# Kernel optimization log

Measured on AMD Instinct MI355X. Metric: run time of the kernel, lower is better.

Reference implementation:

```python
import jax, jax.numpy as jnp
import numpy as np

B, T, C = 4, 1024, 2048
H, N = 32, 64
D_DECAY, D_AAA, D_MV, D_GATE = 96, 96, 64, 256


def setup_inputs() -> dict:
    key = jax.random.key(0)
    ks = iter(jax.random.split(key, 48))

    def rn(shape, s):
        return jax.random.normal(next(ks), shape, jnp.float32) * s

    inp = {
        "x": rn((B, T, C), 1.0),
        "shift_state_in": rn((B, C), 1.0),
        "wkv_state_in": jnp.zeros((B, H, N, N), jnp.float32),
        "v_first_val": rn((B, T, C), 1.0),
    }
    for nme in ["x_r", "x_w", "x_k", "x_v", "x_a", "x_g"]:
        inp[nme] = rn((C,), 0.2) + 0.5
    inp["w0"] = rn((C,), 0.3) - 4.0  # log-log decay bias, keeps decay in (0,1)
    inp["w1"] = rn((C, D_DECAY), 0.02)
    inp["w2"] = rn((D_DECAY, C), 0.02)
    inp["a0"] = rn((C,), 0.1)
    inp["a1"] = rn((C, D_AAA), 0.02)
    inp["a2"] = rn((D_AAA, C), 0.02)
    inp["v0"] = jnp.ones((C,), jnp.float32)
    inp["v1"] = rn((C, D_MV), 0.02)
    inp["v2"] = rn((D_MV, C), 0.02)
    inp["g1"] = rn((C, D_GATE), 0.02)
    inp["g2"] = rn((D_GATE, C), 0.02)
    inp["k_k"] = jnp.full((C,), 0.85, jnp.float32)
    inp["k_a"] = jnp.ones((C,), jnp.float32)
    inp["r_k"] = rn((H, N), 0.02)
    s = 1.0 / float(np.sqrt(C))
    for nme in ["Wr", "Wk", "Wv", "Wo"]:
        inp[nme] = rn((C, C), s)
    inp["ln_w"] = jnp.ones((C,), jnp.float32)
    inp["ln_b"] = jnp.zeros((C,), jnp.float32)
    return inp


def _forward(x, shift_state_in, wkv_state_in, v_first_val,
             x_r, x_w, x_k, x_v, x_a, x_g,
             w0, w1, w2, a0, a1, a2, v0, v1, v2, g1, g2,
             k_k, k_a, r_k, Wr, Wk, Wv, Wo, ln_w, ln_b):
    Bs, Ts, Cs = x.shape
    shift_state_out = x[:, -1]
    # token shift
    xprev = jnp.concatenate([shift_state_in[:, None, :], x[:, :-1]], axis=1)
    dx = xprev - x
    xr = x + dx * x_r
    xw = x + dx * x_w
    xk = x + dx * x_k
    xv = x + dx * x_v
    xa = x + dx * x_a
    xg = x + dx * x_g
    r = xr @ Wr.T
    k = xk @ Wk.T
    v = xv @ Wv.T
    # soft-clamped log-log decay: w in (-inf, -0.5], decay = exp(-exp(w)) in (0,1)
    w_log = -jax.nn.softplus(-(w0 + jnp.tanh(xw @ w1) @ w2)) - 0.5
    decay = jnp.exp(-jnp.exp(w_log))
    a = jax.nn.sigmoid(a0 + (xa @ a1) @ a2)  # in-context learning rate
    g = jax.nn.sigmoid(xg @ g1) @ g2          # output gate
    # removal key: per-head L2-normalized
    kk = (k * k_k).reshape(Bs, Ts, H, N)
    kk = kk / jnp.maximum(jnp.linalg.norm(kk, axis=-1, keepdims=True), 1e-12)
    kk = kk.reshape(Bs, Ts, Cs)
    k = k * (1.0 + (a - 1.0) * k_a)
    # layer_id > 0: value residual mixing with first-layer values
    v = v + (v_first_val - v) * jax.nn.sigmoid(v0 + (xv @ v1) @ v2)
    v_first_out = v_first_val

    # [B,T,C] -> [T,B,H,N] for scan
    def th(t):
        return t.reshape(Bs, Ts, H, N).transpose(1, 0, 2, 3)

    r_s, w_s, k_s, v_s, kk_s, a_s = map(th, (r, decay, k, v, kk, a))

    def step(state, inp):
        rt, wt, kt, vt, kkt, at = inp  # each [B,H,N]
        # state: [B,H,N_value,N_key]
        sab = jnp.einsum('bhvn,bhn,bhm->bhvm', state, -kkt, kkt * at)
        state = state * wt[:, :, None, :] + sab + vt[..., None] * kt[:, :, None, :]
        yt = jnp.einsum('bhvn,bhn->bhv', state, rt)
        return state, yt

    wkv_state_out, y = jax.lax.scan(step, wkv_state_in, (r_s, w_s, k_s, v_s, kk_s, a_s))
    y = y.transpose(1, 0, 2, 3)  # [B,T,H,N]

    # GroupNorm over each head (eps = 1e-5 * head_size)
    eps = 1e-5 * N
    mu = y.mean(-1, keepdims=True)
    var = y.var(-1, keepdims=True)
    yn = (y - mu) / jnp.sqrt(var + eps)
    yn = yn * ln_w.reshape(H, N) + ln_b.reshape(H, N)
    yn = yn.reshape(Bs, Ts, Cs)

    rr = r.reshape(Bs, Ts, H, N)
    kh = k.reshape(Bs, Ts, H, N)
    vh = v.reshape(Bs, Ts, H, N)
    bonus = ((rr * kh * r_k).sum(-1, keepdims=True) * vh).reshape(Bs, Ts, Cs)
    out = ((yn + bonus) * g) @ Wo.T
    return out, shift_state_out, wkv_state_out, v_first_out


def reference(x, shift_state_in, wkv_state_in, v_first_val,
              x_r, x_w, x_k, x_v, x_a, x_g,
              w0, w1, w2, a0, a1, a2, v0, v1, v2, g1, g2,
              k_k, k_a, r_k, Wr, Wk, Wv, Wo, ln_w, ln_b):
    return _forward(x, shift_state_in, wkv_state_in, v_first_val,
                    x_r, x_w, x_k, x_v, x_a, x_g,
                    w0, w1, w2, a0, a1, a2, v0, v1, v2, g1, g2,
                    k_k, k_a, r_k, Wr, Wk, Wv, Wo, ln_w, ln_b)
```

## Files before the change

kernel.cpp:

```cpp
#include <hip/hip_runtime.h>
#include <hip/hip_bf16.h>
#include <stdint.h>

typedef unsigned short u16;
typedef unsigned int u32;
typedef unsigned long long u64;
typedef __attribute__((ext_vector_type(8))) short short8;
typedef __attribute__((ext_vector_type(4))) float f32x4;
typedef __attribute__((ext_vector_type(2))) unsigned int u32x2;

#define BB 4
#define TT 1024
#define CC 2048

__device__ __forceinline__ u16 f2bf(float f){
  __hip_bfloat16 h = __float2bfloat16(f);
  return *reinterpret_cast<u16*>(&h);
}
__device__ __forceinline__ float bf2f(u16 h){
  union { u32 u; float f; } v; v.u = ((u32)h) << 16; return v.f;
}
__device__ __forceinline__ float bflo(u32 p){
  union { u32 u; float f; } v; v.u = p << 16; return v.f;
}
__device__ __forceinline__ float bfhi(u32 p){
  union { u32 u; float f; } v; v.u = p & 0xFFFF0000u; return v.f;
}

__device__ __forceinline__ void gload16(const void* g, void* s){
  __builtin_amdgcn_global_load_lds((const __attribute__((address_space(1))) u32*)g,
                                   (__attribute__((address_space(3))) u32*)s, 16, 0, 0);
}

__device__ __forceinline__ float wave_sum64(float x){
  #pragma unroll
  for (int m = 1; m < 64; m <<= 1) x += __shfl_xor(x, m, 64);
  return x;
}

template<int N>
__device__ __forceinline__ float ror_add(float x){
  int t = __builtin_amdgcn_update_dpp(0, __builtin_bit_cast(int, x), 0x120 | N, 0xF, 0xF, false);
  return x + __builtin_bit_cast(float, t);
}
__device__ __forceinline__ float red16(float x){
  x = ror_add<8>(x); x = ror_add<4>(x); x = ror_add<2>(x); x = ror_add<1>(x);
  return x;
}

__device__ __forceinline__ void xcd_map(int nx, int& bx, int& row0){
  const int G = gridDim.x;
  const int q = G >> 3, r = G & 7;
  const int xcd = blockIdx.x & 7, i2 = blockIdx.x >> 3;
  const int sw = (xcd < r) ? (xcd*(q+1) + i2) : (r*(q+1) + (xcd - r)*q + i2);
  const int by = sw / nx;
  bx = sw - by*nx;
  row0 = by * 128;
}

__global__ __launch_bounds__(256) void k_wprep(
  const float* __restrict__ wr, const float* __restrict__ wk,
  const float* __restrict__ wv, const float* __restrict__ wo,
  const float* __restrict__ w1, const float* __restrict__ a1,
  const float* __restrict__ v1, const float* __restrict__ g1,
  const float* __restrict__ w2, const float* __restrict__ a2,
  const float* __restrict__ v2, const float* __restrict__ g2,
  u16* __restrict__ wsb)
{
  __shared__ float lds[32][33];
  const int blk0 = blockIdx.x;
  if (blk0 < 16384){
    int i = blk0*256 + threadIdx.x;
    int seg = i >> 20;
    int off = (i & 1048575) * 4;
    const float* src = (seg==0) ? wr : (seg==1) ? wk : (seg==2) ? wv : wo;
    const size_t dofs = (seg==0) ? 4194304u : (seg==1) ? 8388608u : (seg==2) ? 12582912u : 0u;
    float4 v = *(const float4*)&src[off];
    *(ushort4*)&wsb[dofs + off] = make_ushort4(f2bf(v.x), f2bf(v.y), f2bf(v.z), f2bf(v.w));
    return;
  }
  const int blk = blk0 - 16384;
  const float* src; int R, S, Rpad, tile, tiles_r; size_t dst;
  if      (blk <  256){ src=w1; R=2048; S=96;   Rpad=2048; dst=16777216u; tile=blk;      tiles_r=64; }
  else if (blk <  512){ src=a1; R=2048; S=96;   Rpad=2048; dst=17039360u; tile=blk-256;  tiles_r=64; }
  else if (blk <  768){ src=v1; R=2048; S=64;   Rpad=2048; dst=17301504u; tile=blk-512;  tiles_r=64; }
  else if (blk < 1280){ src=g1; R=2048; S=256;  Rpad=2048; dst=17563648u; tile=blk-768;  tiles_r=64; }
  else if (blk < 1536){ src=w2; R=96;   S=2048; Rpad=128;  dst=18087936u; tile=blk-1280; tiles_r=4;  }
  else if (blk < 1792){ src=a2; R=96;   S=2048; Rpad=128;  dst=18350080u; tile=blk-1536; tiles_r=4;  }
  else if (blk < 2048){ src=v2; R=64;   S=2048; Rpad=128;  dst=18612224u; tile=blk-1792; tiles_r=4;  }
  else                { src=g2; R=256;  S=2048; Rpad=256;  dst=18874368u; tile=blk-2048; tiles_r=8;  }
  const int tr = tile % tiles_r, ts = tile / tiles_r;
  const int r0 = tr*32, s0 = ts*32;
  const int tj = threadIdx.x & 31, ti = threadIdx.x >> 5;
  #pragma unroll
  for (int p=0;p<4;p++){
    int rr = r0 + p*8 + ti, ss = s0 + tj;
    lds[p*8+ti][tj] = (rr < R && ss < S) ? src[(size_t)rr*S + ss] : 0.f;
  }
  __syncthreads();
  #pragma unroll
  for (int p=0;p<4;p++){
    int sl = p*8 + ti, rl = tj;
    wsb[dst + (size_t)(s0+sl)*Rpad + r0 + rl] = f2bf(lds[rl][sl]);
  }
}

__global__ __launch_bounds__(256) void k_prep4(
  const float* __restrict__ x, const float* __restrict__ shift_in,
  const float* __restrict__ mr, const float* __restrict__ mk,
  const float* __restrict__ mv, const float* __restrict__ mw,
  u16* __restrict__ xr, u16* __restrict__ xk, u16* __restrict__ xv, u16* __restrict__ xw)
{
  int idx = blockIdx.x*256 + threadIdx.x;
  int c4 = (idx & 511) * 4;
  int t  = (idx >> 9) & (TT-1);
  int b  = idx >> 19;
  size_t xo = ((size_t)(b*TT + t))*CC + c4;
  float4 xc = *(const float4*)&x[xo];
  float4 xp = (t == 0) ? *(const float4*)&shift_in[(size_t)b*CC + c4]
                       : *(const float4*)&x[xo - CC];
  float d0 = xp.x-xc.x, d1 = xp.y-xc.y, d2 = xp.z-xc.z, d3 = xp.w-xc.w;
#define MIXO(mp, op) { float4 m = *(const float4*)&mp[c4]; \
    *(ushort4*)&op[xo] = make_ushort4(f2bf(fmaf(d0,m.x,xc.x)), f2bf(fmaf(d1,m.y,xc.y)), \
                                      f2bf(fmaf(d2,m.z,xc.z)), f2bf(fmaf(d3,m.w,xc.w))); }
  MIXO(mr, xr); MIXO(mk, xk); MIXO(mv, xv); MIXO(mw, xw);
#undef MIXO
}

template<int AMODE>
__device__ __forceinline__ void gemm_body(
  const u16* __restrict__ Abf,
  const float* __restrict__ xg, const float* __restrict__ shiftg,
  const float* __restrict__ ma, const float* __restrict__ mg,
  const u16* __restrict__ Bt, float* __restrict__ Cf, u16* __restrict__ Cb,
  int K, int lda, int ldb, int ldc, int nx)
{
  __shared__ alignas(16) u16 sA[128*32];
  __shared__ alignas(16) u16 sB[128*32];
  const int tid = threadIdx.x;
  const int wv = tid >> 6, ln = tid & 63;
  int bx, row0;
  xcd_map(nx, bx, row0);
  const int wr = wv >> 1, wc = wv & 1;

  const float* mixv = nullptr;
  const u16* Ap = Abf;
  const u16* Btp = Bt;
  u16* Cbp = Cb;
  bool bmix = false;
  int bcol0 = bx * 128;
  int ccol0 = bx * 128;
  int ldaa = lda, ldbb = ldb, ldcc = ldc;
  int KK = K, act = 0;

  if (AMODE == 2){
    if (bx < 48){
      int sel = bx >> 4;
      Ap = Abf + (size_t)sel * 8388608u;
      Cbp = Cb + (size_t)sel * 8388608u;
      ccol0 = (bx & 15) * 128;
      ldcc = 2048; ldaa = 2048;
    } else {
      int sb = bx - 48;
      Cbp = (u16*)Cf;
      ccol0 = sb * 128;
      ldcc = 640;
      act = (sb==0) ? 1 : (sb>=3 ? 2 : 0);
      if (sb == 0){ Ap = Abf + 25165824u; ldaa = 2048; }
      else if (sb == 2){ Ap = Abf + 16777216u; ldaa = 2048; }
      else { bmix = true; mixv = (sb==1) ? ma : mg; }
    }
  }
  if (AMODE == 3){
    int sel = bx >> 4;
    Ap = Abf + sel*128;
    Btp = Bt + (size_t)sel * 262144u;
    ldbb = (sel==3) ? 256 : 128;
    KK = (sel==3) ? 256 : 128;
    const int coffs[4] = {0, 8388608, 17842176, 26230784};
    Cbp = Cb + coffs[sel];
    ccol0 = (bx & 15) * 128;
    bcol0 = ccol0;
    ldcc = 2048;
  }

  f32x4 acc[4][4] = {};
  const int ob0 = wv*2048;
  const int o0  = ob0 + ln*16;
  const int rA0 = o0 >> 6;
  const int ke0 = (o0 & 63) >> 1;
  const int ar  = tid >> 2;
  const int akc = (tid & 3) * 8;

  for (int k0 = 0; k0 < KK; k0 += 32){
    __syncthreads();
    if (AMODE != 2 || !bmix){
      gload16(&Ap[(size_t)(row0 + rA0     )*ldaa + k0 + ke0], (void*)((char*)sA + ob0));
      gload16(&Ap[(size_t)(row0 + rA0 + 16)*ldaa + k0 + ke0], (void*)((char*)sA + ob0 + 1024));
    }
    gload16(&Btp[(size_t)(bcol0 + rA0     )*ldbb + k0 + ke0], (void*)((char*)sB + ob0));
    gload16(&Btp[(size_t)(bcol0 + rA0 + 16)*ldbb + k0 + ke0], (void*)((char*)sB + ob0 + 1024));
    if (AMODE == 2 && bmix){
      float4 m0 = *(const float4*)&mixv[k0 + akc];
      float4 m1 = *(const float4*)&mixv[k0 + akc + 4];
      #pragma unroll
      for (int it = 0; it < 2; ++it){
        int r = ar + it*64;
        int gr = row0 + r;
        size_t xo = (size_t)gr*CC + k0 + akc;
        float4 c0 = *(const float4*)&xg[xo];
        float4 c1 = *(const float4*)&xg[xo + 4];
        const float* pp = ((gr & (TT-1)) == 0) ? &shiftg[(size_t)(gr >> 10)*CC + k0 + akc]
                                               : &xg[xo - CC];
        float4 p0 = *(const float4*)&pp[0];
        float4 p1 = *(const float4*)&pp[4];
        short8 vvv;
        vvv[0] = (short)f2bf(c0.x + (p0.x - c0.x)*m0.x);
        vvv[1] = (short)f2bf(c0.y + (p0.y - c0.y)*m0.y);
        vvv[2] = (short)f2bf(c0.z + (p0.z - c0.z)*m0.z);
        vvv[3] = (short)f2bf(c0.w + (p0.w - c0.w)*m0.w);
        vvv[4] = (short)f2bf(c1.x + (p1.x - c1.x)*m1.x);
        vvv[5] = (short)f2bf(c1.y + (p1.y - c1.y)*m1.y);
        vvv[6] = (short)f2bf(c1.z + (p1.z - c1.z)*m1.z);
        vvv[7] = (short)f2bf(c1.w + (p1.w - c1.w)*m1.w);
        *(short8*)&sA[r*32 + akc] = vvv;
      }
    }
    __syncthreads();
    short8 aF[4], bF[4];
    #pragma unroll
    for (int m=0;m<4;m++) aF[m] = *(const short8*)&sA[(wr*64 + m*16 + (ln&15))*32 + (ln>>4)*8];
    #pragma unroll
    for (int n=0;n<4;n++) bF[n] = *(const short8*)&sB[(wc*64 + n*16 + (ln&15))*32 + (ln>>4)*8];
    #pragma unroll
    for (int m=0;m<4;m++)
      #pragma unroll
      for (int n=0;n<4;n++)
        acc[m][n] = __builtin_amdgcn_mfma_f32_16x16x32_bf16(aF[m], bF[n], acc[m][n], 0,0,0);
  }

  const int cr = (ln >> 4) * 4, ccol = ln & 15;
  #pragma unroll
  for (int m=0;m<4;m++){
    #pragma unroll
    for (int n=0;n<4;n++){
      int gc = ccol0 + wc*64 + n*16 + ccol;
      #pragma unroll
      for (int j=0;j<4;j++){
        int gr = row0 + wr*64 + m*16 + cr + j;
        float v = acc[m][n][j];
        if (AMODE == 0){
          Cf[(size_t)gr*ldcc + gc] = v;
        } else {
          if (act == 1) v = tanhf(v);
          else if (act == 2) v = 1.f/(1.f + expf(-v));
          Cbp[(size_t)gr*ldcc + gc] = f2bf(v);
        }
      }
    }
  }
}

__global__ __launch_bounds__(256) void k_gemm_rkv(
  const u16* Abf, const float* xg, const float* shiftg, const float* ma, const float* mg,
  const u16* Bt, float* Cf, u16* Cb, int K, int lda, int ldb, int ldc, int nx)
{ gemm_body<2>(Abf, xg, shiftg, ma, mg, Bt, Cf, Cb, K, lda, ldb, ldc, nx); }

__global__ __launch_bounds__(256) void k_gemm_s2(
  const u16* Abf, const float* xg, const float* shiftg, const float* ma, const float* mg,
  const u16* Bt, float* Cf, u16* Cb, int K, int lda, int ldb, int ldc, int nx)
{ gemm_body<3>(Abf, xg, shiftg, ma, mg, Bt, Cf, Cb, K, lda, ldb, ldc, nx); }

__global__ __launch_bounds__(256) void k_gemm_fin(
  const u16* Abf, const float* xg, const float* shiftg, const float* ma, const float* mg,
  const u16* Bt, float* Cf, u16* Cb, int K, int lda, int ldb, int ldc, int nx)
{ gemm_body<0>(Abf, xg, shiftg, ma, mg, Bt, Cf, Cb, K, lda, ldb, ldc, nx); }

__global__ __launch_bounds__(256) void k_post1(
  u16* __restrict__ kb, u16* __restrict__ vb, const u16* __restrict__ winb,
  u16* __restrict__ ainb, u16* __restrict__ vinb,
  const float* __restrict__ vfirst,
  const float* __restrict__ w0, const float* __restrict__ a0, const float* __restrict__ v0,
  const float* __restrict__ kkv, const float* __restrict__ kav,
  float* __restrict__ dec)
{
  int grp = blockIdx.x*4 + (threadIdx.x >> 6);
  int n = threadIdx.x & 63;
  int i = grp >> 5, h = grp & 31;
  int c = h*64 + n;
  size_t idx = (size_t)i*CC + c;
  float k  = bf2f(kb[idx]),  v = bf2f(vb[idx]);
  float wi = bf2f(winb[idx]), ai = bf2f(ainb[idx]), vi = bf2f(vinb[idx]);
  float vf = vfirst[idx];
  float a  = 1.f/(1.f + expf(-(a0[c] + ai)));
  float z  = -(w0[c] + wi);
  float sp = (z > 15.f) ? z : log1pf(expf(z));
  float decay = expf(-expf(-sp - 0.5f));
  float vg = 1.f/(1.f + expf(-(v0[c] + vi)));
  float vfin = v + (vf - v)*vg;
  float kkr = k * kkv[c];
  float ss = wave_sum64(kkr*kkr);
  float kkn = kkr / fmaxf(sqrtf(ss), 1e-12f);
  float kfin = k * (1.f + (a - 1.f)*kav[c]);
  kb[idx] = f2bf(kfin);
  vb[idx] = f2bf(vfin);
  dec[idx] = decay;
  vinb[idx] = f2bf(kkn);
  ainb[idx] = f2bf(-(kkn * a));
}

#define SDECL(S) float4 w##S[8]; u32x2 b##S[8], k##S[8], kk##S[8], r##S[8]; u32 v##S[8];

#define SISSUE(S, t0) do {                                                        \
  _Pragma("unroll")                                                               \
  for (int s_=0; s_<8; ++s_){                                                     \
    u64 ow = (u64)(uintptr_t)&wb [gc0 + (size_t)((t0)+s_)*CC];                    \
    u64 ob = (u64)(uintptr_t)&bbp[gc0 + (size_t)((t0)+s_)*CC];                    \
    u64 ok = (u64)(uintptr_t)&kb [gc0 + (size_t)((t0)+s_)*CC];                    \
    u64 oq = (u64)(uintptr_t)&kkb[gc0 + (size_t)((t0)+s_)*CC];                    \
    u64 orr= (u64)(uintptr_t)&rb [gc0 + (size_t)((t0)+s_)*CC];                    \
    u64 ov = (u64)(uintptr_t)&vb [gv0 + (size_t)((t0)+s_)*CC];                    \
    asm volatile("global_load_dwordx4 %0, %1, off" : "=v"(w##S[s_])  : "v"(ow) : "memory"); \
    asm volatile("global_load_dwordx2 %0, %1, off" : "=v"(b##S[s_])  : "v"(ob) : "memory"); \
    asm volatile("global_load_dwordx2 %0, %1, off" : "=v"(k##S[s_])  : "v"(ok) : "memory"); \
    asm volatile("global_load_dwordx2 %0, %1, off" : "=v"(kk##S[s_]) : "v"(oq) : "memory"); \
    asm volatile("global_load_dwordx2 %0, %1, off" : "=v"(r##S[s_])  : "v"(orr): "memory"); \
    asm volatile("global_load_dword   %0, %1, off" : "=v"(v##S[s_])  : "v"(ov) : "memory"); \
  }                                                                               \
} while(0)

#define SCHUNK(S, t0, CNT) do {                                                   \
  asm volatile("s_waitcnt vmcnt(" #CNT ")" ::: "memory");                         \
  __builtin_amdgcn_sched_barrier(0);                                              \
  _Pragma("unroll")                                                               \
  for (int s_=0; s_<8; ++s_){                                                     \
    const float w_0=w##S[s_].x, w_1=w##S[s_].y, w_2=w##S[s_].z, w_3=w##S[s_].w;   \
    const float b_0=bflo(b##S[s_].x), b_1=bfhi(b##S[s_].x),                       \
                b_2=bflo(b##S[s_].y), b_3=bfhi(b##S[s_].y);                       \
    const float k_0=bflo(k##S[s_].x), k_1=bfhi(k##S[s_].x),                       \
                k_2=bflo(k##S[s_].y), k_3=bfhi(k##S[s_].y);                       \
    const float q_0=bflo(kk##S[s_].x), q_1=bfhi(kk##S[s_].x),                     \
                q_2=bflo(kk##S[s_].y), q_3=bfhi(kk##S[s_].y);                     \
    const float r_0=bflo(r##S[s_].x), r_1=bfhi(r##S[s_].x),                       \
                r_2=bflo(r##S[s_].y), r_3=bfhi(r##S[s_].y);                       \
    const float vv0_ = bflo(v##S[s_]);                                            \
    const float vv1_ = bfhi(v##S[s_]);                                            \
    float p0_ = fmaf(st[0][0],q_0, st[0][1]*q_1) + fmaf(st[0][2],q_2, st[0][3]*q_3); \
    float p1_ = fmaf(st[1][0],q_0, st[1][1]*q_1) + fmaf(st[1][2],q_2, st[1][3]*q_3); \
    p0_ = red16(p0_); p1_ = red16(p1_);                                           \
    st[0][0] = fmaf(st[0][0],w_0, fmaf(p0_,b_0, vv0_*k_0));                       \
    st[0][1] = fmaf(st[0][1],w_1, fmaf(p0_,b_1, vv0_*k_1));                       \
    st[0][2] = fmaf(st[0][2],w_2, fmaf(p0_,b_2, vv0_*k_2));                       \
    st[0][3] = fmaf(st[0][3],w_3, fmaf(p0_,b_3, vv0_*k_3));                       \
    st[1][0] = fmaf(st[1][0],w_0, fmaf(p1_,b_0, vv1_*k_0));                       \
    st[1][1] = fmaf(st[1][1],w_1, fmaf(p1_,b_1, vv1_*k_1));                       \
    st[1][2] = fmaf(st[1][2],w_2, fmaf(p1_,b_2, vv1_*k_2));                       \
    st[1][3] = fmaf(st[1][3],w_3, fmaf(p1_,b_3, vv1_*k_3));                       \
    float y0_ = fmaf(st[0][0],r_0, st[0][1]*r_1) + fmaf(st[0][2],r_2, st[0][3]*r_3); \
    float y1_ = fmaf(st[1][0],r_0, st[1][1]*r_1) + fmaf(st[1][2],r_2, st[1][3]*r_3); \
    y0_ = red16(y0_); y1_ = red16(y1_);                                           \
    if (cg == 0){                                                                 \
      u32 pk_ = (u32)f2bf(y0_) | ((u32)f2bf(y1_) << 16);                          \
      *(u32*)&yb[gv0 + (size_t)((t0)+s_)*CC] = pk_;                               \
    }                                                                             \
  }                                                                               \
} while(0)

__global__ __launch_bounds__(64, 1) void k_scan(
  const u16* __restrict__ rb, const float* __restrict__ wb,
  const u16* __restrict__ kb, const u16* __restrict__ vb,
  const u16* __restrict__ kkb, const u16* __restrict__ bbp,
  const float* __restrict__ wkv_in, u16* __restrict__ yb, float* __restrict__ wkv_out)
{
  const int blk = blockIdx.x;
  const int bh = blk & 127, oct = blk >> 7;
  const int b = bh >> 5, h = bh & 31;
  const int ln = threadIdx.x;
  const int rg = ln >> 4;
  const int cg = ln & 15;
  const int row0 = oct*8 + rg*2;
  const int col0 = cg*4;

  float st[2][4];
  {
    const float* sp0 = &wkv_in[((size_t)bh*64 + row0    )*64 + col0];
    const float* sp1 = &wkv_in[((size_t)bh*64 + row0 + 1)*64 + col0];
    float4 a = *(const float4*)sp0, c = *(const float4*)sp1;
    st[0][0]=a.x; st[0][1]=a.y; st[0][2]=a.z; st[0][3]=a.w;
    st[1][0]=c.x; st[1][1]=c.y; st[1][2]=c.z; st[1][3]=c.w;
  }

  const size_t gc0 = ((size_t)b*TT)*CC + h*64 + col0;
  const size_t gv0 = ((size_t)b*TT)*CC + h*64 + row0;

  SDECL(A) SDECL(B)

  SISSUE(A, 0);
  SISSUE(B, 8);
  SCHUNK(A, 0, 48);
  SISSUE(A, 16);
  SCHUNK(B, 8, 56);
  SISSUE(B, 24);
  for (int c = 1; c < 63; ++c){
    const int t0 = c*16;
    SCHUNK(A, t0, 56);
    SISSUE(A, t0+16);
    SCHUNK(B, t0+8, 56);
    SISSUE(B, t0+24);
  }
  SCHUNK(A, 1008, 56);
  SCHUNK(B, 1016, 0);

  {
    float* wo0 = &wkv_out[((size_t)bh*64 + row0    )*64 + col0];
    float* wo1 = &wkv_out[((size_t)bh*64 + row0 + 1)*64 + col0];
    *(float4*)wo0 = make_float4(st[0][0], st[0][1], st[0][2], st[0][3]);
    *(float4*)wo1 = make_float4(st[1][0], st[1][1], st[1][2], st[1][3]);
  }
}

__global__ __launch_bounds__(256) void k_post2(
  const u16* __restrict__ ybuf, const u16* __restrict__ rbuf,
  const u16* __restrict__ kfb, const u16* __restrict__ vfb,
  const u16* __restrict__ gbuf, const float* __restrict__ rk,
  const float* __restrict__ lnw, const float* __restrict__ lnb, u16* __restrict__ ao)
{
  int grp = blockIdx.x*4 + (threadIdx.x >> 6);
  int n = threadIdx.x & 63;
  int i = grp >> 5, h = grp & 31;
  int c = h*64 + n;
  size_t idx = (size_t)i*CC + c;
  float y = bf2f(ybuf[idx]);
  float s1 = wave_sum64(y);
  float s2 = wave_sum64(y*y);
  float mu = s1 * (1.f/64.f);
  float var = s2 * (1.f/64.f) - mu*mu;
  float yn = (y - mu) * rsqrtf(var + 6.4e-4f) * lnw[c] + lnb[c];
  float rv = bf2f(rbuf[idx]), kv = bf2f(kfb[idx]);
  float s3 = wave_sum64(rv * kv * rk[c]);
  float bonus = s3 * bf2f(vfb[idx]);
  ao[idx] = f2bf((yn + bonus) * bf2f(gbuf[idx]));
}

__global__ __launch_bounds__(256) void k_shift(const float* __restrict__ x, float* __restrict__ so){
  int i = blockIdx.x*256 + threadIdx.x;
  int b = i >> 9, c4 = (i & 511)*4;
  *(float4*)&so[(size_t)b*CC + c4] = *(const float4*)&x[((size_t)(b*TT + TT-1))*CC + c4];
}

extern "C" void kernel_launch(void* const* d_in, const int* in_sizes, int n_in,
                              void* d_out, int out_size, void* d_ws, size_t ws_size,
                              hipStream_t stream)
{
  const float* x        = (const float*)d_in[0];
  const float* shift_in = (const float*)d_in[1];
  const float* wkv_in   = (const float*)d_in[2];
  const float* v_first  = (const float*)d_in[3];
  const float* x_r = (const float*)d_in[4];
  const float* x_w = (const float*)d_in[5];
  const float* x_k = (const float*)d_in[6];
  const float* x_v = (const float*)d_in[7];
  const float* x_a = (const float*)d_in[8];
  const float* x_g = (const float*)d_in[9];
  const float* w0 = (const float*)d_in[10];
  const float* w1 = (const float*)d_in[11];
  const float* w2 = (const float*)d_in[12];
  const float* a0 = (const float*)d_in[13];
  const float* a1 = (const float*)d_in[14];
  const float* a2 = (const float*)d_in[15];
  const float* v0 = (const float*)d_in[16];
  const float* v1 = (const float*)d_in[17];
  const float* v2 = (const float*)d_in[18];
  const float* g1 = (const float*)d_in[19];
  const float* g2 = (const float*)d_in[20];
  const float* k_k = (const float*)d_in[21];
  const float* k_a = (const float*)d_in[22];
  const float* r_k = (const float*)d_in[23];
  const float* Wr = (const float*)d_in[24];
  const float* Wk = (const float*)d_in[25];
  const float* Wv = (const float*)d_in[26];
  const float* Wo = (const float*)d_in[27];
  const float* ln_w = (const float*)d_in[28];
  const float* ln_b = (const float*)d_in[29];

  char* ws = (char*)d_ws;
  u16* WOB  = (u16*)(ws + 0);
  u16* WRB  = (u16*)(ws + 8388608);
  u16* B2W  = (u16*)(ws + 36175872);
  u16* PBUF = (u16*)(ws + 38797312);
  u16* RB   = (u16*)(ws + 44040192);
  u16* KB   = (u16*)(ws + 60817408);
  u16* VB   = (u16*)(ws + 77594624);
  u16* YB   = (u16*)(ws + 94371840);
  float* DEC  = (float*)(ws + 8388608);
  u16* AO   = (u16*)(ws + 8388608);

  float* out       = (float*)d_out;
  float* shift_out = out + 8388608;
  float* wkv_out   = out + 8396800;
  float* vf_out    = out + 8921088;
  u16* XRKV = (u16*)d_out;
  u16* WINb = (u16*)d_out;
  u16* AINb = (u16*)((char*)d_out + 16777216);
  u16* VINb = (u16*)((char*)d_out + 35684352);

  k_wprep<<<18944, 256, 0, stream>>>(Wr, Wk, Wv, Wo, w1, a1, v1, g1, w2, a2, v2, g2, (u16*)ws);

  k_prep4<<<8192, 256, 0, stream>>>(x, shift_in, x_r, x_k, x_v, x_w,
                                    XRKV, XRKV + 8388608u, XRKV + 16777216u, XRKV + 25165824u);

  k_gemm_rkv<<<1696, 256, 0, stream>>>(XRKV, x, shift_in, x_a, x_g,
                                       WRB, (float*)PBUF, RB, 2048, 2048, 2048, 2048, 53);

  k_gemm_s2<<<2048, 256, 0, stream>>>(PBUF, nullptr, nullptr, nullptr, nullptr,
                                      B2W, nullptr, (u16*)d_out, 0, 640, 128, 2048, 64);

  k_post1<<<32768, 256, 0, stream>>>(KB, VB, WINb, AINb, VINb, v_first,
                                     w0, a0, v0, k_k, k_a, DEC);

  k_scan<<<1024, 64, 0, stream>>>(RB, DEC, KB, VB, VINb, AINb, wkv_in, YB, wkv_out);

  k_post2<<<32768, 256, 0, stream>>>(YB, RB, KB, VB, (u16*)((char*)d_out + 52461568),
                                     r_k, ln_w, ln_b, AO);

  k_gemm_fin<<<512, 256, 0, stream>>>(AO, nullptr, nullptr, nullptr, nullptr,
                                      WOB, out, nullptr, 2048, 2048, 2048, 2048, 16);

  k_shift<<<8, 256, 0, stream>>>(x, shift_out);
  hipMemcpyAsync(vf_out, v_first, 33554432, hipMemcpyDeviceToDevice, stream);
}
```

Baseline: 683.9 us.

## Double GEMM K-tile to 64 with XOR-swizzled shared memory layout

Widens the per-iteration K slice of the shared GEMM body from 32 to 64, halving the number of barrier-separated load/compute iterations, and stores A/B tiles in LDS with an XOR swizzle on 16-byte chunks to avoid bank conflicts on fragment reads. The fused token-shift mix path is extended to fill both 32-wide halves with the same swizzle. LDS usage doubles, which may reduce occupancy, and K values of 128/256 still divide evenly.

```diff
diff --git a/kernel.cpp b/kernel.cpp
--- a/kernel.cpp
+++ b/kernel.cpp
@@ -135,8 +135,8 @@
   const u16* __restrict__ Bt, float* __restrict__ Cf, u16* __restrict__ Cb,
   int K, int lda, int ldb, int ldc, int nx)
 {
-  __shared__ alignas(16) u16 sA[128*32];
-  __shared__ alignas(16) u16 sB[128*32];
+  __shared__ alignas(16) u16 sA[128*64];
+  __shared__ alignas(16) u16 sB[128*64];
   const int tid = threadIdx.x;
   const int wv = tid >> 6, ln = tid & 63;
   int bx, row0;
@@ -185,58 +185,75 @@
   }
 
   f32x4 acc[4][4] = {};
-  const int ob0 = wv*2048;
-  const int o0  = ob0 + ln*16;
-  const int rA0 = o0 >> 6;
-  const int ke0 = (o0 & 63) >> 1;
-  const int ar  = tid >> 2;
-  const int akc = (tid & 3) * 8;
-
-  for (int k0 = 0; k0 < KK; k0 += 32){
+  const int srow = ln >> 3;
+  const int scol = ((ln & 7) ^ srow) * 8;
+  const int ob0  = wv * 4096;
+  const int rsw  = (ln & 7) << 3;
+
+  for (int k0 = 0; k0 < KK; k0 += 64){
     __syncthreads();
     if (AMODE != 2 || !bmix){
-      gload16(&Ap[(size_t)(row0 + rA0     )*ldaa + k0 + ke0], (void*)((char*)sA + ob0));
-      gload16(&Ap[(size_t)(row0 + rA0 + 16)*ldaa + k0 + ke0], (void*)((char*)sA + ob0 + 1024));
+      #pragma unroll
+      for (int j=0;j<4;j++)
+        gload16(&Ap[(size_t)(row0 + wv*32 + j*8 + srow)*ldaa + k0 + scol],
+                (void*)((char*)sA + ob0 + j*1024));
     }
-    gload16(&Btp[(size_t)(bcol0 + rA0     )*ldbb + k0 + ke0], (void*)((char*)sB + ob0));
-    gload16(&Btp[(size_t)(bcol0 + rA0 + 16)*ldbb + k0 + ke0], (void*)((char*)sB + ob0 + 1024));
+    #pragma unroll
+    for (int j=0;j<4;j++)
+      gload16(&Btp[(size_t)(bcol0 + wv*32 + j*8 + srow)*ldbb + k0 + scol],
+              (void*)((char*)sB + ob0 + j*1024));
     if (AMODE == 2 && bmix){
-      float4 m0 = *(const float4*)&mixv[k0 + akc];
-      float4 m1 = *(const float4*)&mixv[k0 + akc + 4];
+      const int r_  = tid >> 2;
+      const int akc = (tid & 3) * 8;
       #pragma unroll
-      for (int it = 0; it < 2; ++it){
-        int r = ar + it*64;
-        int gr = row0 + r;
-        size_t xo = (size_t)gr*CC + k0 + akc;
-        float4 c0 = *(const float4*)&xg[xo];
-        float4 c1 = *(const float4*)&xg[xo + 4];
-        const float* pp = ((gr & (TT-1)) == 0) ? &shiftg[(size_t)(gr >> 10)*CC + k0 + akc]
-                                               : &xg[xo - CC];
-        float4 p0 = *(const float4*)&pp[0];
-        float4 p1 = *(const float4*)&pp[4];
-        short8 vvv;
-        vvv[0] = (short)f2bf(c0.x + (p0.x - c0.x)*m0.x);
-        vvv[1] = (short)f2bf(c0.y + (p0.y - c0.y)*m0.y);
-        vvv[2] = (short)f2bf(c0.z + (p0.z - c0.z)*m0.z);
-        vvv[3] = (short)f2bf(c0.w + (p0.w - c0.w)*m0.w);
-        vvv[4] = (short)f2bf(c1.x + (p1.x - c1.x)*m1.x);
-        vvv[5] = (short)f2bf(c1.y + (p1.y - c1.y)*m1.y);
-        vvv[6] = (short)f2bf(c1.z + (p1.z - c1.z)*m1.z);
-        vvv[7] = (short)f2bf(c1.w + (p1.w - c1.w)*m1.w);
-        *(short8*)&sA[r*32 + akc] = vvv;
+      for (int kb2 = 0; kb2 < 64; kb2 += 32){
+        float4 m0 = *(const float4*)&mixv[k0 + kb2 + akc];
+        float4 m1 = *(const float4*)&mixv[k0 + kb2 + akc + 4];
+        #pragma unroll
+        for (int it = 0; it < 2; ++it){
+          int r = r_ + it*64;
+          int gr = row0 + r;
+          size_t xo = (size_t)gr*CC + k0 + kb2 + akc;
+          float4 c0 = *(const float4*)&xg[xo];
+          float4 c1 = *(const float4*)&xg[xo + 4];
+          const float* pp = ((gr & (TT-1)) == 0) ? &shiftg[(size_t)(gr >> 10)*CC + k0 + kb2 + akc]
+                                                 : &xg[xo - CC];
+          float4 p0 = *(const float4*)&pp[0];
+          float4 p1 = *(const float4*)&pp[4];
+          short8 vvv;
+          vvv[0] = (short)f2bf(c0.x + (p0.x - c0.x)*m0.x);
+          vvv[1] = (short)f2bf(c0.y + (p0.y - c0.y)*m0.y);
+          vvv[2] = (short)f2bf(c0.z + (p0.z - c0.z)*m0.z);
+          vvv[3] = (short)f2bf(c0.w + (p0.w - c0.w)*m0.w);
+          vvv[4] = (short)f2bf(c1.x + (p1.x - c1.x)*m1.x);
+          vvv[5] = (short)f2bf(c1.y + (p1.y - c1.y)*m1.y);
+          vvv[6] = (short)f2bf(c1.z + (p1.z - c1.z)*m1.z);
+          vvv[7] = (short)f2bf(c1.w + (p1.w - c1.w)*m1.w);
+          int csw = (kb2 + akc) ^ ((r & 7) << 3);
+          *(short8*)&sA[r*64 + csw] = vvv;
+        }
       }
     }
     __syncthreads();
-    short8 aF[4], bF[4];
     #pragma unroll
-    for (int m=0;m<4;m++) aF[m] = *(const short8*)&sA[(wr*64 + m*16 + (ln&15))*32 + (ln>>4)*8];
-    #pragma unroll
-    for (int n=0;n<4;n++) bF[n] = *(const short8*)&sB[(wc*64 + n*16 + (ln&15))*32 + (ln>>4)*8];
-    #pragma unroll
-    for (int m=0;m<4;m++)
+    for (int kk = 0; kk < 2; ++kk){
+      short8 aF[4], bF[4];
       #pragma unroll
-      for (int n=0;n<4;n++)
-        acc[m][n] = __builtin_amdgcn_mfma_f32_16x16x32_bf16(aF[m], bF[n], acc[m][n], 0,0,0);
+      for (int m=0;m<4;m++){
+        int rr = wr*64 + m*16 + (ln&15);
+        aF[m] = *(const short8*)&sA[rr*64 + ((kk*32 + (ln>>4)*8) ^ rsw)];
+      }
+      #pragma unroll
+      for (int n=0;n<4;n++){
+        int rr = wc*64 + n*16 + (ln&15);
+        bF[n] = *(const short8*)&sB[rr*64 + ((kk*32 + (ln>>4)*8) ^ rsw)];
+      }
+      #pragma unroll
+      for (int m=0;m<4;m++)
+        #pragma unroll
+        for (int n=0;n<4;n++)
+          acc[m][n] = __builtin_amdgcn_mfma_f32_16x16x32_bf16(aF[m], bF[n], acc[m][n], 0,0,0);
+    }
   }
 
   const int cr = (ln >> 4) * 4, ccol = ln & 15;
```

Result: faster. 666.5 us (-2.5%).
